# Kernel tuning notes

Measured on AMD Instinct MI355X. Metric: run time of the kernel, lower is better.

## Reference

```python
import jax, jax.numpy as jnp
import numpy as np


def setup_inputs() -> dict:
    key = jax.random.key(0)
    ks = jax.random.split(key, 6)
    B, C, W, H = 8, 512, 64, 64
    return {
        "x": jax.random.normal(ks[0], (B, C, W, H), dtype=jnp.float32),
        "proj_query": jax.random.normal(ks[1], (C, W, H), dtype=jnp.float32),
        "key_w": jax.random.normal(ks[2], (C, C), dtype=jnp.float32) * 0.02,
        "key_b": jax.random.normal(ks[3], (C,), dtype=jnp.float32) * 0.02,
        "value_w": jax.random.normal(ks[4], (C, C), dtype=jnp.float32) * 0.02,
        "value_b": jax.random.normal(ks[5], (C,), dtype=jnp.float32) * 0.02,
        "gamma": jnp.ones((1,), dtype=jnp.float32),
    }


def reference(x, proj_query, key_w, key_b, value_w, value_b, gamma):
    B, C, W, H = x.shape
    N = W * H
    # fixed memory query: (C, N); torch builds B x N x C via permute
    q = proj_query.reshape(C, N)
    # 1x1 convs == per-pixel channel matmuls
    k = jnp.einsum('oc,bchw->bohw', key_w, x) + key_b[None, :, None, None]
    v = jnp.einsum('oc,bchw->bohw', value_w, x) + value_b[None, :, None, None]
    k = k.reshape(B, C, N)
    v = v.reshape(B, C, N)
    # energy = bmm(key [B,C,N], query^T [N,C]) -> B x C x C (channel attention)
    energy = jnp.einsum('bcn,dn->bcd', k, q)
    attention = jax.nn.softmax(energy, axis=-1)
    # out = bmm(attention^T [B,C,C], value [B,C,N]) -> B x C x N
    out = jnp.einsum('bdc,bdn->bcn', attention, v)
    out = out.reshape(B, C, W, H)
    return gamma * out + x
```

## Files before the change

### kernel.cpp

```cpp
#include <hip/hip_runtime.h>

typedef unsigned short u16;
typedef unsigned int u32;
typedef unsigned long long u64;
typedef _Float16 f16x8 __attribute__((ext_vector_type(8)));
typedef float f32x4 __attribute__((ext_vector_type(4)));

__device__ __forceinline__ u16 f2h(float f) {
  union { _Float16 h; u16 u; } c; c.h = (_Float16)f; return c.u;
}
__device__ __forceinline__ float h2f(u16 v) {
  union { u16 u; _Float16 h; } c; c.u = v; return (float)c.h;
}

__device__ __forceinline__ f32x4 mfma16(f16x8 a, f16x8 b, f32x4 c) {
  return __builtin_amdgcn_mfma_f32_16x16x32_f16(a, b, c, 0, 0, 0);
}

__device__ __forceinline__ void ld8f(const float* s, u16* o) {
  float4 a = *(const float4*)s;
  float4 b = *(const float4*)(s + 4);
  o[0] = f2h(a.x); o[1] = f2h(a.y); o[2] = f2h(a.z); o[3] = f2h(a.w);
  o[4] = f2h(b.x); o[5] = f2h(b.y); o[6] = f2h(b.z); o[7] = f2h(b.w);
}

__device__ __forceinline__ void glds16(const u16* g, u16* l) {
  __builtin_amdgcn_global_load_lds(
      reinterpret_cast<const __attribute__((address_space(1))) u32*>(reinterpret_cast<u64>(g)),
      reinterpret_cast<__attribute__((address_space(3))) u32*>(reinterpret_cast<u64>(l)),
      16, 0, 0);
}

template<int TM, int TN, bool NNB>
__device__ __forceinline__ void gemm_core(const u16* __restrict__ A, int lda,
                                          const u16* __restrict__ B, int ldb,
                                          int ksteps, u16* sA, u16* sB, f32x4 acc[TM][TN]) {
  const int t = threadIdx.x;
  const int lane = t & 63, wave = t >> 6;
  const int wm = wave >> 1, wn = wave & 1;
  const int m16 = lane & 15, q4 = lane >> 4;
  constexpr int BM = TM * 32, BN = TN * 32;
  constexpr int TILEA = BM * 32, TILEB = BN * 32;
  constexpr int APF = BM / 64;
  constexpr int BPF = BN / 64;
  constexpr int VPI = NNB ? (APF + 2) : (APF + BPF);

  int aoff[APF], asl[APF];
#pragma unroll
  for (int p = 0; p < APF; ++p) {
    int s = p * 256 + t, row = s >> 2;
    int kc = (s & 3) ^ ((row >> 1) & 3);
    aoff[p] = row * lda + kc * 8;
    asl[p] = (p * 256 + (t & 192)) * 8;
  }
  int boff[BPF], bsl[BPF];
  if constexpr (!NNB) {
#pragma unroll
    for (int p = 0; p < BPF; ++p) {
      int s = p * 256 + t, row = s >> 2;
      int kc = (s & 3) ^ ((row >> 1) & 3);
      boff[p] = row * ldb + kc * 8;
      bsl[p] = (p * 256 + (t & 192)) * 8;
    }
  }

  int aro[TM], bro[TN];
#pragma unroll
  for (int i = 0; i < TM; ++i) {
    int row = wm * TM * 16 + i * 16 + m16;
    aro[i] = row * 32 + ((q4 ^ ((row >> 1) & 3)) << 3);
  }
#pragma unroll
  for (int j = 0; j < TN; ++j) {
    int row = wn * TN * 16 + j * 16 + m16;
    bro[j] = row * 32 + ((q4 ^ ((row >> 1) & 3)) << 3);
  }

  const int bkk = (t >> 4) * 2;
  const int bnn = (t & 15) * 8;
  const int bpar = (t >> 2) & 1;
  int bwo[8];
  if constexpr (NNB) {
#pragma unroll
    for (int ee = 0; ee < 8; ++ee) {
      int n = bnn + (ee ^ bpar);
      bwo[ee] = n * 32 + (((bkk >> 3) ^ ((n >> 1) & 3)) << 3) + (bkk & 7);
    }
  }

  u16 *aR = sA, *aS = sA + TILEA, *aT = sA + 2 * TILEA;
  u16 *bR = sB, *bS = sB + TILEB, *bT = sB + 2 * TILEB;

  int4 nb0, nb1;
  if constexpr (NNB) {
    const u16* src = B + (size_t)bkk * ldb + bnn;
    nb0 = *(const int4*)src;
    nb1 = *(const int4*)(src + ldb);
    __builtin_amdgcn_sched_barrier(0);
  }
#pragma unroll
  for (int p = 0; p < APF; ++p) glds16(A + aoff[p], aR + asl[p]);
  if constexpr (!NNB) {
#pragma unroll
    for (int p = 0; p < BPF; ++p) glds16(B + boff[p], bR + bsl[p]);
  } else {
    union { int4 v; u16 h[8]; } u0, u1; u0.v = nb0; u1.v = nb1;
    u32 val[8];
#pragma unroll
    for (int e = 0; e < 8; ++e) val[e] = (u32)u0.h[e] | ((u32)u1.h[e] << 16);
#pragma unroll
    for (int ee = 0; ee < 8; ++ee)
      *(u32*)&bR[bwo[ee]] = bpar ? val[ee ^ 1] : val[ee];
  }

#pragma unroll 1
  for (int kt = 0; kt < ksteps; ++kt) {
    const bool more = kt + 1 < ksteps;

    if (more) {
      if constexpr (NNB) {
        const u16* src = B + ((size_t)(kt + 1) * 32 + bkk) * ldb + bnn;
        nb0 = *(const int4*)src;
        nb1 = *(const int4*)(src + ldb);
        __builtin_amdgcn_sched_barrier(0);
      }
      const u16* An = A + (kt + 1) * 32;
#pragma unroll
      for (int p = 0; p < APF; ++p) glds16(An + aoff[p], aS + asl[p]);
      if constexpr (!NNB) {
        const u16* Bn = B + (kt + 1) * 32;
#pragma unroll
        for (int p = 0; p < BPF; ++p) glds16(Bn + boff[p], bS + bsl[p]);
      }
      if constexpr (NNB)
        asm volatile("s_waitcnt vmcnt(%0) lgkmcnt(0)" :: "n"(VPI) : "memory");
      else
        asm volatile("s_waitcnt vmcnt(%0)" :: "n"(VPI) : "memory");
    } else {
      if constexpr (NNB)
        asm volatile("s_waitcnt vmcnt(0) lgkmcnt(0)" ::: "memory");
      else
        asm volatile("s_waitcnt vmcnt(0)" ::: "memory");
    }
    __builtin_amdgcn_s_barrier();
    __builtin_amdgcn_sched_barrier(0);

    f16x8 af[TM], bv[TN];
#pragma unroll
    for (int i = 0; i < TM; ++i) af[i] = *(const f16x8*)&aR[aro[i]];
#pragma unroll
    for (int j = 0; j < TN; ++j) bv[j] = *(const f16x8*)&bR[bro[j]];
#pragma unroll
    for (int i = 0; i < TM; ++i)
#pragma unroll
      for (int j = 0; j < TN; ++j)
        acc[i][j] = mfma16(af[i], bv[j], acc[i][j]);

    if constexpr (NNB) {
      if (more) {
        union { int4 v; u16 h[8]; } u0, u1; u0.v = nb0; u1.v = nb1;
        u32 val[8];
#pragma unroll
        for (int e = 0; e < 8; ++e) val[e] = (u32)u0.h[e] | ((u32)u1.h[e] << 16);
#pragma unroll
        for (int ee = 0; ee < 8; ++ee)
          *(u32*)&bS[bwo[ee]] = bpar ? val[ee ^ 1] : val[ee];
      }
    }

    { u16* x = aR; aR = aS; aS = aT; aT = x; }
    if constexpr (!NNB) { u16* x = bR; bR = bS; bS = bT; bT = x; }
    else               { u16* x = bR; bR = bS; bS = x; }
  }
}

__global__ __launch_bounds__(256) void cvt_x_kernel(const float* __restrict__ x, u16* __restrict__ xh) {
  size_t i = ((size_t)blockIdx.x * 256 + threadIdx.x) * 8;
  u16 o[8];
  ld8f(x + i, o);
  *(int4*)&xh[i] = *(int4*)o;
}

__global__ __launch_bounds__(256) void cvt_q_kernel(const float* __restrict__ q, u16* __restrict__ qh,
                                                    float* __restrict__ qs) {
  int row = blockIdx.x, t = threadIdx.x;
  float s = 0.f;
#pragma unroll
  for (int p = 0; p < 2; ++p) {
    size_t i = (size_t)row * 4096 + p * 2048 + t * 8;
    u16 o[8];
    ld8f(q + i, o);
#pragma unroll
    for (int e = 0; e < 8; ++e) s += h2f(o[e]);
    *(int4*)&qh[i] = *(int4*)o;
  }
  for (int off = 32; off; off >>= 1) s += __shfl_xor(s, off);
  __shared__ float wsum[4];
  if ((t & 63) == 0) wsum[t >> 6] = s;
  __syncthreads();
  if (t == 0) qs[row] = wsum[0] + wsum[1] + wsum[2] + wsum[3];
}

__global__ __launch_bounds__(256) void prep_kernel(const float* __restrict__ vw, u16* __restrict__ vwT,
                                                   const float* __restrict__ kw, u16* __restrict__ kwh,
                                                   float* __restrict__ beta) {
  int blk = blockIdx.x, t = threadIdx.x;
  if (blk < 256) {
    __shared__ u16 sT[32 * 33];
    int bx = blk & 15, by = blk >> 4;
#pragma unroll
    for (int p = 0; p < 4; ++p) {
      int idx = p * 256 + t; int r = idx >> 5, c = idx & 31;
      sT[r * 33 + c] = f2h(vw[(size_t)(by * 32 + r) * 512 + bx * 32 + c]);
    }
    __syncthreads();
#pragma unroll
    for (int p = 0; p < 4; ++p) {
      int idx = p * 256 + t; int r = idx >> 5, c = idx & 31;
      vwT[(size_t)(bx * 32 + r) * 512 + by * 32 + c] = sT[c * 33 + r];
    }
  } else if (blk < 384) {
    size_t i = ((size_t)(blk - 256) * 256 + t) * 8;
    u16 o[8];
    ld8f(kw + i, o);
    *(int4*)&kwh[i] = *(int4*)o;
  } else {
    for (int i = t; i < 4096; i += 256) beta[i] = 0.f;
  }
}

__global__ __launch_bounds__(256) void sgemm_kernel(const u16* __restrict__ qh, const u16* __restrict__ xh,
                                                    u16* __restrict__ Sh) {
  __shared__ __align__(16) u16 sA[3 * 64 * 32], sB[3 * 64 * 32];
  int rt = blockIdx.x, jt = blockIdx.y;
  f32x4 acc[2][2];
#pragma unroll
  for (int i = 0; i < 2; ++i)
#pragma unroll
    for (int j = 0; j < 2; ++j) acc[i][j] = (f32x4){0.f, 0.f, 0.f, 0.f};
  gemm_core<2, 2, false>(qh + (size_t)jt * 64 * 4096, 4096,
                         xh + (size_t)rt * 64 * 4096, 4096, 128, sA, sB, acc);

  const int t = threadIdx.x, lane = t & 63, wave = t >> 6;
  const int wm = wave >> 1, wn = wave & 1, m16 = lane & 15, q4 = lane >> 4;
  int b = (rt * 64) >> 9, o0 = (rt * 64) & 511;
  u16* Ob = Sh + (size_t)b * 262144;
#pragma unroll
  for (int i = 0; i < 2; ++i)
#pragma unroll
    for (int j = 0; j < 2; ++j)
#pragma unroll
      for (int r = 0; r < 4; ++r) {
        int y = jt * 64 + wm * 32 + i * 16 + q4 * 4 + r;
        int o = o0 + wn * 32 + j * 16 + m16;
        Ob[(size_t)y * 512 + o] = f2h(acc[i][j][r]);
      }
}

__global__ __launch_bounds__(256) void egemm_kernel(const u16* __restrict__ kwh, const u16* __restrict__ Sh,
                                                    float* __restrict__ E) {
  __shared__ __align__(16) u16 sA[3 * 64 * 32], sB[3 * 64 * 32];
  int xt = blockIdx.x >> 3, yt = blockIdx.x & 7, b = blockIdx.y;
  f32x4 acc[2][2];
#pragma unroll
  for (int i = 0; i < 2; ++i)
#pragma unroll
    for (int j = 0; j < 2; ++j) acc[i][j] = (f32x4){0.f, 0.f, 0.f, 0.f};
  gemm_core<2, 2, false>(kwh + (size_t)xt * 64 * 512, 512,
                         Sh + (size_t)b * 262144 + (size_t)yt * 64 * 512, 512, 16, sA, sB, acc);

  const int t = threadIdx.x, lane = t & 63, wave = t >> 6;
  const int wm = wave >> 1, wn = wave & 1, m16 = lane & 15, q4 = lane >> 4;
  float* O = E + ((size_t)b * 512 + xt * 64) * 512 + yt * 64;
#pragma unroll
  for (int i = 0; i < 2; ++i)
#pragma unroll
    for (int j = 0; j < 2; ++j)
#pragma unroll
      for (int r = 0; r < 4; ++r) {
        int row = wm * 32 + i * 16 + q4 * 4 + r;
        int col = wn * 32 + j * 16 + m16;
        O[(size_t)row * 512 + col] = acc[i][j][r];
      }
}

__global__ __launch_bounds__(256) void softmax_kernel(const float* __restrict__ E, const float* __restrict__ qs,
                                                      const float* __restrict__ kb, const float* __restrict__ vb,
                                                      u16* __restrict__ attT, float* __restrict__ beta) {
  __shared__ float sE[16 * 516];
  __shared__ float sM[16], sS[16];
  int i0 = blockIdx.x * 16, b = blockIdx.y, t = threadIdx.x;
  const float* Eb = E + ((size_t)b * 512 + i0) * 512;
  for (int ch = 0; ch < 32; ++ch) {
    int idx = ch * 256 + t;
    int row = idx >> 9, col = idx & 511;
    sE[row * 516 + col] = Eb[(size_t)row * 512 + col] + kb[i0 + row] * qs[col];
  }
  __syncthreads();
  {
    int row = t >> 4, sub = t & 15;
    float mx = -1e30f;
    for (int ii = 0; ii < 32; ++ii) mx = fmaxf(mx, sE[row * 516 + sub + ii * 16]);
    for (int off = 8; off; off >>= 1) mx = fmaxf(mx, __shfl_xor(mx, off));
    float sm = 0.f;
    for (int ii = 0; ii < 32; ++ii) sm += __expf(sE[row * 516 + sub + ii * 16] - mx);
    for (int off = 8; off; off >>= 1) sm += __shfl_xor(sm, off);
    if (sub == 0) { sM[row] = mx; sS[row] = 1.f / sm; }
  }
  __syncthreads();
  float vbr = vb[i0 + (t & 15)];
  u16* Ob = attT + (size_t)b * 262144;
  for (int ch = 0; ch < 32; ++ch) {
    int idx = ch * 256 + t;
    int r = idx & 15, j = idx >> 4;
    float a = __expf(sE[r * 516 + j] - sM[r]) * sS[r];
    Ob[(size_t)j * 512 + i0 + r] = f2h(a);
    float part = a * vbr;
    for (int off = 8; off; off >>= 1) part += __shfl_xor(part, off);
    if (r == 0) atomicAdd(&beta[b * 512 + j], part);
  }
}

__global__ __launch_bounds__(256) void wgemm_kernel(const u16* __restrict__ attT, const u16* __restrict__ vwT,
                                                    u16* __restrict__ W) {
  __shared__ __align__(16) u16 sA[3 * 64 * 32], sB[3 * 64 * 32];
  int ct = blockIdx.x >> 3, ot = blockIdx.x & 7, b = blockIdx.y;
  f32x4 acc[2][2];
#pragma unroll
  for (int i = 0; i < 2; ++i)
#pragma unroll
    for (int j = 0; j < 2; ++j) acc[i][j] = (f32x4){0.f, 0.f, 0.f, 0.f};
  gemm_core<2, 2, false>(attT + (size_t)b * 262144 + (size_t)ct * 64 * 512, 512,
                         vwT + (size_t)ot * 64 * 512, 512, 16, sA, sB, acc);

  const int t = threadIdx.x, lane = t & 63, wave = t >> 6;
  const int wm = wave >> 1, wn = wave & 1, m16 = lane & 15, q4 = lane >> 4;
  u16* O = W + (size_t)b * 262144 + (size_t)(ct * 64) * 512 + ot * 64;
#pragma unroll
  for (int i = 0; i < 2; ++i)
#pragma unroll
    for (int j = 0; j < 2; ++j)
#pragma unroll
      for (int r = 0; r < 4; ++r) {
        int row = wm * 32 + i * 16 + q4 * 4 + r;
        int col = wn * 32 + j * 16 + m16;
        O[(size_t)row * 512 + col] = f2h(acc[i][j][r]);
      }
}

__global__ __launch_bounds__(256) void outgemm_kernel(const u16* __restrict__ W, const u16* __restrict__ xh,
                                                      const float* __restrict__ x, const float* __restrict__ beta,
                                                      const float* __restrict__ gm, float* __restrict__ out) {
  __shared__ __align__(16) u16 sA[3 * 128 * 32], sB[2 * 128 * 32];
  int nt = blockIdx.x, ct = blockIdx.y, b = blockIdx.z;
  f32x4 acc[4][4];
#pragma unroll
  for (int i = 0; i < 4; ++i)
#pragma unroll
    for (int j = 0; j < 4; ++j) acc[i][j] = (f32x4){0.f, 0.f, 0.f, 0.f};
  gemm_core<4, 4, true>(W + (size_t)b * 262144 + (size_t)ct * 128 * 512, 512,
                        xh + (size_t)b * 2097152 + nt * 128, 4096, 16, sA, sB, acc);

  const int t = threadIdx.x, lane = t & 63, wave = t >> 6;
  const int wm = wave >> 1, wn = wave & 1, m16 = lane & 15, q4 = lane >> 4;
  float g = gm[0];
#pragma unroll
  for (int i = 0; i < 4; ++i)
#pragma unroll
    for (int j = 0; j < 4; ++j)
#pragma unroll
      for (int r = 0; r < 4; ++r) {
        int c = ct * 128 + wm * 64 + i * 16 + q4 * 4 + r;
        int n = nt * 128 + wn * 64 + j * 16 + m16;
        size_t idx = (size_t)b * 2097152 + (size_t)c * 4096 + n;
        out[idx] = g * (acc[i][j][r] + beta[b * 512 + c]) + x[idx];
      }
}

extern "C" void kernel_launch(void* const* d_in, const int* in_sizes, int n_in,
                              void* d_out, int out_size, void* d_ws, size_t ws_size,
                              hipStream_t stream) {
  const float* x  = (const float*)d_in[0];
  const float* pq = (const float*)d_in[1];
  const float* kw = (const float*)d_in[2];
  const float* kb = (const float*)d_in[3];
  const float* vw = (const float*)d_in[4];
  const float* vb = (const float*)d_in[5];
  const float* gm = (const float*)d_in[6];
  float* out = (float*)d_out;

  char* ws = (char*)d_ws;
  u16*   xh   = (u16*)(ws);
  u16*   qh   = (u16*)(ws + (32ull << 20));
  u16*   Sh   = (u16*)(ws + (36ull << 20));
  u16*   W    = (u16*)(ws + (36ull << 20));
  float* E    = (float*)(ws + (40ull << 20));
  u16*   attT = (u16*)(ws + (48ull << 20));
  u16*   kwh  = (u16*)(ws + (52ull << 20));
  u16*   vwT  = (u16*)(ws + (52ull << 20) + 524288);
  char*  sm   = ws + (53ull << 20);
  float* qs   = (float*)(sm);
  float* beta = (float*)(sm + 4096);

  cvt_x_kernel<<<dim3(8192), 256, 0, stream>>>(x, xh);
  cvt_q_kernel<<<dim3(512), 256, 0, stream>>>(pq, qh, qs);
  prep_kernel<<<dim3(385), 256, 0, stream>>>(vw, vwT, kw, kwh, beta);
  sgemm_kernel<<<dim3(64, 8), 256, 0, stream>>>(qh, xh, Sh);
  egemm_kernel<<<dim3(64, 8), 256, 0, stream>>>(kwh, Sh, E);
  softmax_kernel<<<dim3(32, 8), 256, 0, stream>>>(E, qs, kb, vb, attT, beta);
  wgemm_kernel<<<dim3(64, 8), 256, 0, stream>>>(attT, vwT, W);
  outgemm_kernel<<<dim3(32, 4, 8), 256, 0, stream>>>(W, xh, x, beta, gm, out);
}
```

Before: 238.6 us.

## Pre-transpose x to N-major fp16 so out GEMM uses async LDS loads for B

The x conversion kernel now also writes a transposed fp16 copy (N x C per batch) through an LDS transpose. The output GEMM reads that copy, so its B operand loads directly into LDS with global_load_lds and triple buffering, like the other GEMMs. This replaces the old register-staged load and in-register transpose path (NNB). The cost is an extra 32 MB fp16 write in the conversion kernel and a larger LDS footprint in the output GEMM.

```diff
diff --git a/kernel.cpp b/kernel.cpp
--- a/kernel.cpp
+++ b/kernel.cpp
@@ -31,7 +31,7 @@
       16, 0, 0);
 }
 
-template<int TM, int TN, bool NNB>
+template<int TM, int TN>
 __device__ __forceinline__ void gemm_core(const u16* __restrict__ A, int lda,
                                           const u16* __restrict__ B, int ldb,
                                           int ksteps, u16* sA, u16* sB, f32x4 acc[TM][TN]) {
@@ -41,9 +41,8 @@
   const int m16 = lane & 15, q4 = lane >> 4;
   constexpr int BM = TM * 32, BN = TN * 32;
   constexpr int TILEA = BM * 32, TILEB = BN * 32;
-  constexpr int APF = BM / 64;
-  constexpr int BPF = BN / 64;
-  constexpr int VPI = NNB ? (APF + 2) : (APF + BPF);
+  constexpr int APF = BM / 64, BPF = BN / 64;
+  constexpr int VPI = APF + BPF;
 
   int aoff[APF], asl[APF];
 #pragma unroll
@@ -54,14 +53,12 @@
     asl[p] = (p * 256 + (t & 192)) * 8;
   }
   int boff[BPF], bsl[BPF];
-  if constexpr (!NNB) {
-#pragma unroll
-    for (int p = 0; p < BPF; ++p) {
-      int s = p * 256 + t, row = s >> 2;
-      int kc = (s & 3) ^ ((row >> 1) & 3);
-      boff[p] = row * ldb + kc * 8;
-      bsl[p] = (p * 256 + (t & 192)) * 8;
-    }
+#pragma unroll
+  for (int p = 0; p < BPF; ++p) {
+    int s = p * 256 + t, row = s >> 2;
+    int kc = (s & 3) ^ ((row >> 1) & 3);
+    boff[p] = row * ldb + kc * 8;
+    bsl[p] = (p * 256 + (t & 192)) * 8;
   }
 
   int aro[TM], bro[TN];
@@ -76,71 +73,28 @@
     bro[j] = row * 32 + ((q4 ^ ((row >> 1) & 3)) << 3);
   }
 
-  const int bkk = (t >> 4) * 2;
-  const int bnn = (t & 15) * 8;
-  const int bpar = (t >> 2) & 1;
-  int bwo[8];
-  if constexpr (NNB) {
-#pragma unroll
-    for (int ee = 0; ee < 8; ++ee) {
-      int n = bnn + (ee ^ bpar);
-      bwo[ee] = n * 32 + (((bkk >> 3) ^ ((n >> 1) & 3)) << 3) + (bkk & 7);
-    }
-  }
-
   u16 *aR = sA, *aS = sA + TILEA, *aT = sA + 2 * TILEA;
   u16 *bR = sB, *bS = sB + TILEB, *bT = sB + 2 * TILEB;
 
-  int4 nb0, nb1;
-  if constexpr (NNB) {
-    const u16* src = B + (size_t)bkk * ldb + bnn;
-    nb0 = *(const int4*)src;
-    nb1 = *(const int4*)(src + ldb);
-    __builtin_amdgcn_sched_barrier(0);
-  }
 #pragma unroll
   for (int p = 0; p < APF; ++p) glds16(A + aoff[p], aR + asl[p]);
-  if constexpr (!NNB) {
-#pragma unroll
-    for (int p = 0; p < BPF; ++p) glds16(B + boff[p], bR + bsl[p]);
-  } else {
-    union { int4 v; u16 h[8]; } u0, u1; u0.v = nb0; u1.v = nb1;
-    u32 val[8];
-#pragma unroll
-    for (int e = 0; e < 8; ++e) val[e] = (u32)u0.h[e] | ((u32)u1.h[e] << 16);
-#pragma unroll
-    for (int ee = 0; ee < 8; ++ee)
-      *(u32*)&bR[bwo[ee]] = bpar ? val[ee ^ 1] : val[ee];
-  }
+#pragma unroll
+  for (int p = 0; p < BPF; ++p) glds16(B + boff[p], bR + bsl[p]);
 
 #pragma unroll 1
   for (int kt = 0; kt < ksteps; ++kt) {
     const bool more = kt + 1 < ksteps;
 
     if (more) {
-      if constexpr (NNB) {
-        const u16* src = B + ((size_t)(kt + 1) * 32 + bkk) * ldb + bnn;
-        nb0 = *(const int4*)src;
-        nb1 = *(const int4*)(src + ldb);
-        __builtin_amdgcn_sched_barrier(0);
-      }
       const u16* An = A + (kt + 1) * 32;
 #pragma unroll
       for (int p = 0; p < APF; ++p) glds16(An + aoff[p], aS + asl[p]);
-      if constexpr (!NNB) {
-        const u16* Bn = B + (kt + 1) * 32;
-#pragma unroll
-        for (int p = 0; p < BPF; ++p) glds16(Bn + boff[p], bS + bsl[p]);
-      }
-      if constexpr (NNB)
-        asm volatile("s_waitcnt vmcnt(%0) lgkmcnt(0)" :: "n"(VPI) : "memory");
-      else
-        asm volatile("s_waitcnt vmcnt(%0)" :: "n"(VPI) : "memory");
+      const u16* Bn = B + (kt + 1) * 32;
+#pragma unroll
+      for (int p = 0; p < BPF; ++p) glds16(Bn + boff[p], bS + bsl[p]);
+      asm volatile("s_waitcnt vmcnt(%0)" :: "n"(VPI) : "memory");
     } else {
-      if constexpr (NNB)
-        asm volatile("s_waitcnt vmcnt(0) lgkmcnt(0)" ::: "memory");
-      else
-        asm volatile("s_waitcnt vmcnt(0)" ::: "memory");
+      asm volatile("s_waitcnt vmcnt(0)" ::: "memory");
     }
     __builtin_amdgcn_s_barrier();
     __builtin_amdgcn_sched_barrier(0);
@@ -156,29 +110,41 @@
       for (int j = 0; j < TN; ++j)
         acc[i][j] = mfma16(af[i], bv[j], acc[i][j]);
 
-    if constexpr (NNB) {
-      if (more) {
-        union { int4 v; u16 h[8]; } u0, u1; u0.v = nb0; u1.v = nb1;
-        u32 val[8];
-#pragma unroll
-        for (int e = 0; e < 8; ++e) val[e] = (u32)u0.h[e] | ((u32)u1.h[e] << 16);
-#pragma unroll
-        for (int ee = 0; ee < 8; ++ee)
-          *(u32*)&bS[bwo[ee]] = bpar ? val[ee ^ 1] : val[ee];
-      }
-    }
-
     { u16* x = aR; aR = aS; aS = aT; aT = x; }
-    if constexpr (!NNB) { u16* x = bR; bR = bS; bS = bT; bT = x; }
-    else               { u16* x = bR; bR = bS; bS = x; }
-  }
-}
-
-__global__ __launch_bounds__(256) void cvt_x_kernel(const float* __restrict__ x, u16* __restrict__ xh) {
-  size_t i = ((size_t)blockIdx.x * 256 + threadIdx.x) * 8;
-  u16 o[8];
-  ld8f(x + i, o);
-  *(int4*)&xh[i] = *(int4*)o;
+    { u16* x = bR; bR = bS; bS = bT; bT = x; }
+  }
+}
+
+__global__ __launch_bounds__(256) void cvt_xt_kernel(const float* __restrict__ x,
+                                                     u16* __restrict__ xh,
+                                                     u16* __restrict__ xhT) {
+  __shared__ __align__(16) u16 T[64 * 72];
+  int nt = blockIdx.x, ot = blockIdx.y, b = blockIdx.z;
+  int t = threadIdx.x;
+  int s = t & 31;
+  int c = (t >> 5) * 8;
+
+  const float* xp = x + ((size_t)b * 512 + ot * 64 + 2 * s) * 4096 + nt * 64 + c;
+  u16 r0[8], r1[8];
+  ld8f(xp, r0);
+  ld8f(xp + 4096, r1);
+
+  u16* xq = xh + ((size_t)b * 512 + ot * 64 + 2 * s) * 4096 + nt * 64 + c;
+  *(int4*)xq = *(int4*)r0;
+  *(int4*)(xq + 4096) = *(int4*)r1;
+
+  u32* Tw = (u32*)T;
+#pragma unroll
+  for (int e = 0; e < 8; ++e)
+    Tw[(c + e) * 36 + s] = (u32)r0[e] | ((u32)r1[e] << 16);
+  __syncthreads();
+
+  int rr = t >> 2, og = t & 3;
+  int4 v0 = *(const int4*)&T[rr * 72 + og * 16];
+  int4 v1 = *(const int4*)&T[rr * 72 + og * 16 + 8];
+  u16* xo = xhT + ((size_t)b * 4096 + nt * 64 + rr) * 512 + ot * 64 + og * 16;
+  *(int4*)xo = v0;
+  *(int4*)(xo + 8) = v1;
 }
 
 __global__ __launch_bounds__(256) void cvt_q_kernel(const float* __restrict__ q, u16* __restrict__ qh,
@@ -238,8 +204,8 @@
   for (int i = 0; i < 2; ++i)
 #pragma unroll
     for (int j = 0; j < 2; ++j) acc[i][j] = (f32x4){0.f, 0.f, 0.f, 0.f};
-  gemm_core<2, 2, false>(qh + (size_t)jt * 64 * 4096, 4096,
-                         xh + (size_t)rt * 64 * 4096, 4096, 128, sA, sB, acc);
+  gemm_core<2, 2>(qh + (size_t)jt * 64 * 4096, 4096,
+                  xh + (size_t)rt * 64 * 4096, 4096, 128, sA, sB, acc);
 
   const int t = threadIdx.x, lane = t & 63, wave = t >> 6;
   const int wm = wave >> 1, wn = wave & 1, m16 = lane & 15, q4 = lane >> 4;
@@ -266,8 +232,8 @@
   for (int i = 0; i < 2; ++i)
 #pragma unroll
     for (int j = 0; j < 2; ++j) acc[i][j] = (f32x4){0.f, 0.f, 0.f, 0.f};
-  gemm_core<2, 2, false>(kwh + (size_t)xt * 64 * 512, 512,
-                         Sh + (size_t)b * 262144 + (size_t)yt * 64 * 512, 512, 16, sA, sB, acc);
+  gemm_core<2, 2>(kwh + (size_t)xt * 64 * 512, 512,
+                  Sh + (size_t)b * 262144 + (size_t)yt * 64 * 512, 512, 16, sA, sB, acc);
 
   const int t = threadIdx.x, lane = t & 63, wave = t >> 6;
   const int wm = wave >> 1, wn = wave & 1, m16 = lane & 15, q4 = lane >> 4;
@@ -330,8 +296,8 @@
   for (int i = 0; i < 2; ++i)
 #pragma unroll
     for (int j = 0; j < 2; ++j) acc[i][j] = (f32x4){0.f, 0.f, 0.f, 0.f};
-  gemm_core<2, 2, false>(attT + (size_t)b * 262144 + (size_t)ct * 64 * 512, 512,
-                         vwT + (size_t)ot * 64 * 512, 512, 16, sA, sB, acc);
+  gemm_core<2, 2>(attT + (size_t)b * 262144 + (size_t)ct * 64 * 512, 512,
+                  vwT + (size_t)ot * 64 * 512, 512, 16, sA, sB, acc);
 
   const int t = threadIdx.x, lane = t & 63, wave = t >> 6;
   const int wm = wave >> 1, wn = wave & 1, m16 = lane & 15, q4 = lane >> 4;
@@ -348,18 +314,18 @@
       }
 }
 
-__global__ __launch_bounds__(256) void outgemm_kernel(const u16* __restrict__ W, const u16* __restrict__ xh,
+__global__ __launch_bounds__(256) void outgemm_kernel(const u16* __restrict__ W, const u16* __restrict__ xhT,
                                                       const float* __restrict__ x, const float* __restrict__ beta,
                                                       const float* __restrict__ gm, float* __restrict__ out) {
-  __shared__ __align__(16) u16 sA[3 * 128 * 32], sB[2 * 128 * 32];
+  __shared__ __align__(16) u16 sA[3 * 128 * 32], sB[3 * 128 * 32];
   int nt = blockIdx.x, ct = blockIdx.y, b = blockIdx.z;
   f32x4 acc[4][4];
 #pragma unroll
   for (int i = 0; i < 4; ++i)
 #pragma unroll
     for (int j = 0; j < 4; ++j) acc[i][j] = (f32x4){0.f, 0.f, 0.f, 0.f};
-  gemm_core<4, 4, true>(W + (size_t)b * 262144 + (size_t)ct * 128 * 512, 512,
-                        xh + (size_t)b * 2097152 + nt * 128, 4096, 16, sA, sB, acc);
+  gemm_core<4, 4>(W + (size_t)b * 262144 + (size_t)ct * 128 * 512, 512,
+                  xhT + (size_t)b * 2097152 + (size_t)nt * 128 * 512, 512, 16, sA, sB, acc);
 
   const int t = threadIdx.x, lane = t & 63, wave = t >> 6;
   const int wm = wave >> 1, wn = wave & 1, m16 = lane & 15, q4 = lane >> 4;
@@ -401,13 +367,14 @@
   char*  sm   = ws + (53ull << 20);
   float* qs   = (float*)(sm);
   float* beta = (float*)(sm + 4096);
-
-  cvt_x_kernel<<<dim3(8192), 256, 0, stream>>>(x, xh);
+  u16*   xhT  = (u16*)(ws + (54ull << 20));
+
+  cvt_xt_kernel<<<dim3(64, 8, 8), 256, 0, stream>>>(x, xh, xhT);
   cvt_q_kernel<<<dim3(512), 256, 0, stream>>>(pq, qh, qs);
   prep_kernel<<<dim3(385), 256, 0, stream>>>(vw, vwT, kw, kwh, beta);
   sgemm_kernel<<<dim3(64, 8), 256, 0, stream>>>(qh, xh, Sh);
   egemm_kernel<<<dim3(64, 8), 256, 0, stream>>>(kwh, Sh, E);
   softmax_kernel<<<dim3(32, 8), 256, 0, stream>>>(E, qs, kb, vb, attT, beta);
   wgemm_kernel<<<dim3(64, 8), 256, 0, stream>>>(attT, vwT, W);
-  outgemm_kernel<<<dim3(32, 4, 8), 256, 0, stream>>>(W, xh, x, beta, gm, out);
-}
+  outgemm_kernel<<<dim3(32, 4, 8), 256, 0, stream>>>(W, xhT, x, beta, gm, out);
+}
```

Result: slower. 246.3 us (+3.2%).
